# Optimization experiments

Measured on AMD Instinct MI355X. Metric: run time of the kernel, lower is better.

The kernel has to match this reference:

```python
import jax, jax.numpy as jnp
import numpy as np

B, D, IN_F, OUT_F, BLOCK = 2, 1024, 4096, 4096, 128
N_BLOCKS = IN_F // BLOCK  # 32


def setup_inputs() -> dict:
    key = jax.random.key(0)
    k1, k2, k3 = jax.random.split(key, 3)
    inputs = jax.random.normal(k1, (B, D, IN_F), dtype=jnp.float32)
    # int8 quantized weight buffer: [n_blocks, block_size, out_features]
    weight = jax.random.randint(k2, (N_BLOCKS, BLOCK, OUT_F), -128, 128, dtype=jnp.int32).astype(jnp.int8)
    # per-block, per-output-channel scaler: [n_blocks, out_features]
    weight_scaler = (jax.random.uniform(k3, (N_BLOCKS, OUT_F), dtype=jnp.float32) * 0.01 + 0.001)
    return {"inputs": inputs, "weight": weight, "weight_scaler": weight_scaler}


def reference(inputs, weight, weight_scaler):
    # Faithful port of WeightOnlyBlockwiseQuantizedLinear.blockwise_jax_kernel
    # (default path: symmetric quantization, zero_point is None).
    weight = weight.astype(jnp.int8)
    block_size = weight.shape[1]
    b, d, in_f = inputs.shape
    # [b, d, n_blocks s, block_size c]
    x = inputs.reshape(b, d, in_f // block_size, block_size)
    # per-block int8 matmul (promoted to float32 by x): [b, d, s, z]
    out = jnp.einsum("scz,bdsc->bdsz", weight, x)
    # apply per-block scaler and reduce over blocks: [b, d, z]
    out = jnp.einsum("bdsz,sz->bdz", out, weight_scaler)
    return out
```

## Files before the change

### kernel.cpp

```cpp
#include <hip/hip_runtime.h>
#include <hip/hip_bf16.h>


#define MDIM 2048
#define NDIM 4096
#define KDIM 4096
#define NBLK 32
#define BM 128
#define BN 256
#define BK 64
#define NT (KDIM / BK)

typedef __attribute__((ext_vector_type(8))) short bf16x8;
typedef __attribute__((ext_vector_type(4))) float f32x4;
typedef __attribute__((ext_vector_type(8))) unsigned short u16x8;

__device__ __forceinline__ unsigned short f2bf(float f) {
  unsigned u = __float_as_uint(f);
  u += 0x7fffu + ((u >> 16) & 1u);
  return (unsigned short)(u >> 16);
}

__device__ __forceinline__ void gl_lds16(const void* g, void* l) {
  __builtin_amdgcn_global_load_lds(
      (const __attribute__((address_space(1))) unsigned int*)g,
      (__attribute__((address_space(3))) unsigned int*)l,
      16, 0, 0);
}

__global__ void prep_a_kernel(const float* __restrict__ x,
                              unsigned short* __restrict__ ab) {
  int i = blockIdx.x * blockDim.x + threadIdx.x;
  const float4 v = reinterpret_cast<const float4*>(x)[i];
  ushort4 hv;
  hv.x = f2bf(v.x); hv.y = f2bf(v.y); hv.z = f2bf(v.z); hv.w = f2bf(v.w);
  reinterpret_cast<ushort4*>(ab)[i] = hv;
}

__global__ void prep_b_kernel(const int* __restrict__ w,
                              const float* __restrict__ scaler,
                              unsigned short* __restrict__ bt) {
  __shared__ __align__(16) unsigned short tile[64][72];
  const int t = threadIdx.x;
  const int k0 = blockIdx.y * 64;
  const int n0 = blockIdx.x * 64;
  const int s = k0 >> 7;
  {
    const int kl = t >> 2;
    const int nb = t & 3;
    const int nbase = n0 + nb * 16;
    const int4* src = reinterpret_cast<const int4*>(w + (size_t)(k0 + kl) * NDIM + nbase);
    const float4* scv = reinterpret_cast<const float4*>(scaler + (size_t)s * NDIM + nbase);
#pragma unroll
    for (int q = 0; q < 4; ++q) {
      const int4 v = src[q];
      const float4 sc = scv[q];
      const int rbase = nb * 16 + q * 4;
      const int swzr = ((rbase >> 3) & 7) << 3;
      const int ckl = kl ^ swzr;
      tile[rbase + 0][ckl] = f2bf((float)v.x * sc.x);
      tile[rbase + 1][ckl] = f2bf((float)v.y * sc.y);
      tile[rbase + 2][ckl] = f2bf((float)v.z * sc.z);
      tile[rbase + 3][ckl] = f2bf((float)v.w * sc.w);
    }
  }
  __syncthreads();
  {
    const int nl = t >> 2;
    const int swzn = (nl >> 3) & 7;
#pragma unroll
    for (int q = 0; q < 2; ++q) {
      const int ch = (t & 3) * 2 + q;
      u16x8 v = *reinterpret_cast<const u16x8*>(&tile[nl][(ch ^ swzn) * 8]);
      *reinterpret_cast<u16x8*>(bt + (size_t)(n0 + nl) * KDIM + k0 + ch * 8) = v;
    }
  }
}

#define MFMA_BF16 __builtin_amdgcn_mfma_f32_16x16x32_bf16

__global__ __launch_bounds__(512, 2)
void gemm_kernel(const unsigned short* __restrict__ ab,
                 const unsigned short* __restrict__ bt,
                 float* __restrict__ out) {
  __shared__ __align__(16) char lds[98304];

  const int t = threadIdx.x;
  const int lane = t & 63;
  const int wid = t >> 6;
  const int wm = wid >> 2;
  const int wn = wid & 3;
  const int lane15 = lane & 15;
  const int laneq = lane >> 4;
  const int swz = (lane & 7) << 4;

  const unsigned flat = blockIdx.x;
  const unsigned swzb = (flat & 7u) * 32u + (flat >> 3);
  const int ntile = swzb & 15;
  const int mtile = swzb >> 4;
  const int m0 = mtile * BM;
  const int n0 = ntile * BN;

  const int srow = t >> 3;
  const int sslot = (t & 7) ^ (srow & 7);
  const char* ga = (const char*)ab + ((size_t)(m0 + srow) * KDIM) * 2 + sslot * 16;
  const char* gb = (const char*)bt + ((size_t)(n0 + srow) * KDIM) * 2 + sslot * 16;
  const size_t rstep = (size_t)64 * KDIM * 2;

  char* const lA0 = lds + (size_t)wid * 1024;
  char* const lB0 = lds + 32768 + (size_t)wid * 1024;

#define STAGE(kt, c) do {                                   \
    const size_t ko_ = (size_t)(kt) * (BK * 2);             \
    char* a_ = lA0 + (c) * 16384;                           \
    char* b_ = lB0 + (c) * 32768;                           \
    gl_lds16(ga + ko_,             a_);                     \
    gl_lds16(ga + ko_ + rstep,     a_ + 8192);              \
    gl_lds16(gb + ko_,             b_);                     \
    gl_lds16(gb + ko_ + rstep,     b_ + 8192);              \
    gl_lds16(gb + ko_ + 2 * rstep, b_ + 16384);             \
    gl_lds16(gb + ko_ + 3 * rstep, b_ + 24576);             \
  } while (0)

  int offA[4], offB[4];
#pragma unroll
  for (int i = 0; i < 4; ++i) {
    offA[i] = (wm * 64 + i * 16 + lane15) * 128 + laneq * 16;
    offB[i] = (wn * 64 + i * 16 + lane15) * 128 + laneq * 16;
  }

  const f32x4 fzero = {0.f, 0.f, 0.f, 0.f};
  f32x4 acc[4][4];
#pragma unroll
  for (int m = 0; m < 4; ++m)
#pragma unroll
    for (int n = 0; n < 4; ++n) acc[m][n] = fzero;

  STAGE(0, 0);
  STAGE(1, 1);
  asm volatile("s_waitcnt vmcnt(6)" ::: "memory");
  __builtin_amdgcn_s_barrier();

#define LDA(m, base) do {                                             \
    af[m][0] = *(const bf16x8*)((base) + ((offA[m]) ^ swz));          \
    af[m][1] = *(const bf16x8*)((base) + ((offA[m] + 64) ^ swz));     \
  } while (0)
#define LDB(n, base) do {                                             \
    bfr[n][0] = *(const bf16x8*)((base) + ((offB[n]) ^ swz));         \
    bfr[n][1] = *(const bf16x8*)((base) + ((offB[n] + 64) ^ swz));    \
  } while (0)
#define QUAD(mA, mB, nA, nB) do {                                     \
    __builtin_amdgcn_s_setprio(1);                                    \
    acc[mA][nA] = MFMA_BF16(af[mA][0], bfr[nA][0], acc[mA][nA], 0, 0, 0); \
    acc[mA][nB] = MFMA_BF16(af[mA][0], bfr[nB][0], acc[mA][nB], 0, 0, 0); \
    acc[mB][nA] = MFMA_BF16(af[mB][0], bfr[nA][0], acc[mB][nA], 0, 0, 0); \
    acc[mB][nB] = MFMA_BF16(af[mB][0], bfr[nB][0], acc[mB][nB], 0, 0, 0); \
    acc[mA][nA] = MFMA_BF16(af[mA][1], bfr[nA][1], acc[mA][nA], 0, 0, 0); \
    acc[mA][nB] = MFMA_BF16(af[mA][1], bfr[nB][1], acc[mA][nB], 0, 0, 0); \
    acc[mB][nA] = MFMA_BF16(af[mB][1], bfr[nA][1], acc[mB][nA], 0, 0, 0); \
    acc[mB][nB] = MFMA_BF16(af[mB][1], bfr[nB][1], acc[mB][nB], 0, 0, 0); \
    __builtin_amdgcn_s_setprio(0);                                    \
  } while (0)

#pragma unroll 2
  for (int t2 = 0; t2 < NT; ++t2) {
    const int c = t2 & 1;
    const char* lac = lds + c * 16384;
    const char* lbc = lds + 32768 + c * 32768;
    bf16x8 af[4][2], bfr[4][2];

    LDA(0, lac); LDA(1, lac); LDB(0, lbc); LDB(1, lbc);
    __builtin_amdgcn_s_barrier();
    QUAD(0, 1, 0, 1);
    __builtin_amdgcn_s_barrier();

    LDB(2, lbc); LDB(3, lbc);
    __builtin_amdgcn_s_barrier();
    QUAD(0, 1, 2, 3);
    __builtin_amdgcn_s_barrier();

    LDA(2, lac); LDA(3, lac);
    __builtin_amdgcn_s_barrier();
    QUAD(2, 3, 2, 3);
    __builtin_amdgcn_s_barrier();
    __builtin_amdgcn_sched_barrier(0);

    if (t2 + 2 < NT) STAGE(t2 + 2, c);
    QUAD(2, 3, 0, 1);
    if (t2 + 2 < NT) {
      asm volatile("s_waitcnt vmcnt(6)" ::: "memory");
    } else {
      asm volatile("s_waitcnt vmcnt(0)" ::: "memory");
    }
    __builtin_amdgcn_s_barrier();
  }

#pragma unroll
  for (int m = 0; m < 4; ++m)
#pragma unroll
    for (int r = 0; r < 4; ++r) {
      const int row = m0 + wm * 64 + m * 16 + laneq * 4 + r;
      float* op = out + (size_t)row * NDIM + n0 + wn * 64 + lane15;
#pragma unroll
      for (int n = 0; n < 4; ++n) op[n * 16] = acc[m][n][r];
    }
#undef STAGE
#undef LDA
#undef LDB
#undef QUAD
}

__global__ void fallback_kernel(const float* __restrict__ x,
                                const int* __restrict__ w,
                                const float* __restrict__ scaler,
                                float* __restrict__ out) {
  const int n = blockIdx.x * 256 + threadIdx.x;
  const int m = blockIdx.y;
  float acc = 0.f;
  for (int s = 0; s < NBLK; ++s) {
    float p = 0.f;
    const float* xr = x + (size_t)m * KDIM + s * 128;
    const int* wr = w + (size_t)s * 128 * NDIM + n;
#pragma unroll 8
    for (int c = 0; c < 128; ++c) p += xr[c] * (float)wr[(size_t)c * NDIM];
    acc += p * scaler[s * NDIM + n];
  }
  out[(size_t)m * NDIM + n] = acc;
}

extern "C" void kernel_launch(void* const* d_in, const int* in_sizes, int n_in,
                              void* d_out, int out_size, void* d_ws, size_t ws_size,
                              hipStream_t stream) {
  (void)in_sizes; (void)n_in; (void)out_size;
  const float* x = (const float*)d_in[0];
  const int* w = (const int*)d_in[1];
  const float* sc = (const float*)d_in[2];
  float* out = (float*)d_out;

  const size_t need = (size_t)51 * 1024 * 1024;
  if (ws_size >= need) {
    unsigned short* ab = (unsigned short*)d_ws;
    unsigned short* bt = ab + (size_t)MDIM * KDIM;
    prep_a_kernel<<<(MDIM * KDIM / 4) / 256, 256, 0, stream>>>(x, ab);
    prep_b_kernel<<<dim3(NDIM / 64, KDIM / 64), 256, 0, stream>>>(w, sc, bt);
    gemm_kernel<<<(MDIM / BM) * (NDIM / BN), 512, 0, stream>>>(ab, bt, out);
  } else {
    fallback_kernel<<<dim3(NDIM / 256, MDIM), 256, 0, stream>>>(x, w, sc, out);
  }
}
```

Before: 203.8 us.

## Register-transpose weight prep and software-pipeline LDS fragment loads in GEMM

```diff
diff --git a/kernel.cpp b/kernel.cpp
--- a/kernel.cpp
+++ b/kernel.cpp
@@ -40,41 +40,32 @@
 __global__ void prep_b_kernel(const int* __restrict__ w,
                               const float* __restrict__ scaler,
                               unsigned short* __restrict__ bt) {
-  __shared__ __align__(16) unsigned short tile[64][72];
   const int t = threadIdx.x;
-  const int k0 = blockIdx.y * 64;
-  const int n0 = blockIdx.x * 64;
-  const int s = k0 >> 7;
+  const int n0 = blockIdx.x * 128;
+  const int k0 = blockIdx.y * 128;
+  const int s = blockIdx.y;
+  const int k8 = (t & 15) * 8;
+  const int n8 = (t >> 4) * 8;
+
+  float sc[8];
   {
-    const int kl = t >> 2;
-    const int nb = t & 3;
-    const int nbase = n0 + nb * 16;
-    const int4* src = reinterpret_cast<const int4*>(w + (size_t)(k0 + kl) * NDIM + nbase);
-    const float4* scv = reinterpret_cast<const float4*>(scaler + (size_t)s * NDIM + nbase);
-#pragma unroll
-    for (int q = 0; q < 4; ++q) {
-      const int4 v = src[q];
-      const float4 sc = scv[q];
-      const int rbase = nb * 16 + q * 4;
-      const int swzr = ((rbase >> 3) & 7) << 3;
-      const int ckl = kl ^ swzr;
-      tile[rbase + 0][ckl] = f2bf((float)v.x * sc.x);
-      tile[rbase + 1][ckl] = f2bf((float)v.y * sc.y);
-      tile[rbase + 2][ckl] = f2bf((float)v.z * sc.z);
-      tile[rbase + 3][ckl] = f2bf((float)v.w * sc.w);
-    }
-  }
-  __syncthreads();
-  {
-    const int nl = t >> 2;
-    const int swzn = (nl >> 3) & 7;
-#pragma unroll
-    for (int q = 0; q < 2; ++q) {
-      const int ch = (t & 3) * 2 + q;
-      u16x8 v = *reinterpret_cast<const u16x8*>(&tile[nl][(ch ^ swzn) * 8]);
-      *reinterpret_cast<u16x8*>(bt + (size_t)(n0 + nl) * KDIM + k0 + ch * 8) = v;
-    }
-  }
+    const float4* scv = reinterpret_cast<const float4*>(scaler + (size_t)s * NDIM + n0 + n8);
+    const float4 s0 = scv[0], s1 = scv[1];
+    sc[0] = s0.x; sc[1] = s0.y; sc[2] = s0.z; sc[3] = s0.w;
+    sc[4] = s1.x; sc[5] = s1.y; sc[6] = s1.z; sc[7] = s1.w;
+  }
+  u16x8 outv[8];
+#pragma unroll
+  for (int r = 0; r < 8; ++r) {
+    const int4* src = reinterpret_cast<const int4*>(w + (size_t)(k0 + k8 + r) * NDIM + n0 + n8);
+    const int4 a = src[0], b = src[1];
+    const int v[8] = {a.x, a.y, a.z, a.w, b.x, b.y, b.z, b.w};
+#pragma unroll
+    for (int j = 0; j < 8; ++j) outv[j][r] = f2bf((float)v[j] * sc[j]);
+  }
+#pragma unroll
+  for (int j = 0; j < 8; ++j)
+    *reinterpret_cast<u16x8*>(bt + (size_t)(n0 + n8 + j) * KDIM + k0 + k8) = outv[j];
 }
 
 #define MFMA_BF16 __builtin_amdgcn_mfma_f32_16x16x32_bf16
@@ -136,63 +127,82 @@
 #pragma unroll
     for (int n = 0; n < 4; ++n) acc[m][n] = fzero;
 
+  bf16x8 af[4][2];
+  bf16x8 bfr[2][4][2];
+
+#define LDA(m, base) do {                                             \
+    af[m][0] = *(const bf16x8*)((base) + ((offA[m]) ^ swz));          \
+    af[m][1] = *(const bf16x8*)((base) + ((offA[m] + 64) ^ swz));     \
+  } while (0)
+#define LDB(S, n, base) do {                                          \
+    bfr[S][n][0] = *(const bf16x8*)((base) + ((offB[n]) ^ swz));      \
+    bfr[S][n][1] = *(const bf16x8*)((base) + ((offB[n] + 64) ^ swz)); \
+  } while (0)
+#define HALF(mA, mB, P) do {                                               \
+    acc[mA][0] = MFMA_BF16(af[mA][0], bfr[P][0][0], acc[mA][0], 0, 0, 0);  \
+    acc[mA][1] = MFMA_BF16(af[mA][0], bfr[P][1][0], acc[mA][1], 0, 0, 0);  \
+    acc[mA][2] = MFMA_BF16(af[mA][0], bfr[P][2][0], acc[mA][2], 0, 0, 0);  \
+    acc[mA][3] = MFMA_BF16(af[mA][0], bfr[P][3][0], acc[mA][3], 0, 0, 0);  \
+    acc[mB][0] = MFMA_BF16(af[mB][0], bfr[P][0][0], acc[mB][0], 0, 0, 0);  \
+    acc[mB][1] = MFMA_BF16(af[mB][0], bfr[P][1][0], acc[mB][1], 0, 0, 0);  \
+    acc[mB][2] = MFMA_BF16(af[mB][0], bfr[P][2][0], acc[mB][2], 0, 0, 0);  \
+    acc[mB][3] = MFMA_BF16(af[mB][0], bfr[P][3][0], acc[mB][3], 0, 0, 0);  \
+    acc[mA][0] = MFMA_BF16(af[mA][1], bfr[P][0][1], acc[mA][0], 0, 0, 0);  \
+    acc[mA][1] = MFMA_BF16(af[mA][1], bfr[P][1][1], acc[mA][1], 0, 0, 0);  \
+    acc[mA][2] = MFMA_BF16(af[mA][1], bfr[P][2][1], acc[mA][2], 0, 0, 0);  \
+    acc[mA][3] = MFMA_BF16(af[mA][1], bfr[P][3][1], acc[mA][3], 0, 0, 0);  \
+    acc[mB][0] = MFMA_BF16(af[mB][1], bfr[P][0][1], acc[mB][0], 0, 0, 0);  \
+    acc[mB][1] = MFMA_BF16(af[mB][1], bfr[P][1][1], acc[mB][1], 0, 0, 0);  \
+    acc[mB][2] = MFMA_BF16(af[mB][1], bfr[P][2][1], acc[mB][2], 0, 0, 0);  \
+    acc[mB][3] = MFMA_BF16(af[mB][1], bfr[P][3][1], acc[mB][3], 0, 0, 0);  \
+  } while (0)
+
+#define BODY(t2, P) do {                                                   \
+    char* lac = lds + (P) * 16384;                                         \
+                                                        \
+    LDA(2, lac); LDA(3, lac);                                              \
+    __builtin_amdgcn_s_barrier();                                          \
+    __builtin_amdgcn_s_setprio(1);                                         \
+    HALF(0, 1, P);                                                         \
+    __builtin_amdgcn_s_setprio(0);                                         \
+    asm volatile("s_waitcnt lgkmcnt(0)" ::: "memory"); \
+    __builtin_amdgcn_s_barrier();                                          \
+                                                        \
+    if ((t2) + 2 < NT) {                                                   \
+      STAGE((t2) + 2, P);                                                  \
+      asm volatile("s_waitcnt vmcnt(6)" ::: "memory");    \
+    } else {                                                               \
+      asm volatile("s_waitcnt vmcnt(0)" ::: "memory");                     \
+    }                                                                      \
+    __builtin_amdgcn_s_barrier();                                          \
+    __builtin_amdgcn_sched_barrier(0);                                     \
+    if ((t2) + 1 < NT) {                                                   \
+      char* nac = lds + (1 - (P)) * 16384;                                 \
+      char* nbc = lds + 32768 + (1 - (P)) * 32768;                         \
+      LDA(0, nac); LDA(1, nac);                                            \
+      LDB(1 - (P), 0, nbc); LDB(1 - (P), 1, nbc);                          \
+      LDB(1 - (P), 2, nbc); LDB(1 - (P), 3, nbc);                          \
+    }                                                                      \
+    __builtin_amdgcn_s_setprio(1);                                         \
+    HALF(2, 3, P);                                                         \
+    __builtin_amdgcn_s_setprio(0);                                         \
+    __builtin_amdgcn_s_barrier();                                          \
+  } while (0)
+
   STAGE(0, 0);
   STAGE(1, 1);
   asm volatile("s_waitcnt vmcnt(6)" ::: "memory");
   __builtin_amdgcn_s_barrier();
-
-#define LDA(m, base) do {                                             \
-    af[m][0] = *(const bf16x8*)((base) + ((offA[m]) ^ swz));          \
-    af[m][1] = *(const bf16x8*)((base) + ((offA[m] + 64) ^ swz));     \
-  } while (0)
-#define LDB(n, base) do {                                             \
-    bfr[n][0] = *(const bf16x8*)((base) + ((offB[n]) ^ swz));         \
-    bfr[n][1] = *(const bf16x8*)((base) + ((offB[n] + 64) ^ swz));    \
-  } while (0)
-#define QUAD(mA, mB, nA, nB) do {                                     \
-    __builtin_amdgcn_s_setprio(1);                                    \
-    acc[mA][nA] = MFMA_BF16(af[mA][0], bfr[nA][0], acc[mA][nA], 0, 0, 0); \
-    acc[mA][nB] = MFMA_BF16(af[mA][0], bfr[nB][0], acc[mA][nB], 0, 0, 0); \
-    acc[mB][nA] = MFMA_BF16(af[mB][0], bfr[nA][0], acc[mB][nA], 0, 0, 0); \
-    acc[mB][nB] = MFMA_BF16(af[mB][0], bfr[nB][0], acc[mB][nB], 0, 0, 0); \
-    acc[mA][nA] = MFMA_BF16(af[mA][1], bfr[nA][1], acc[mA][nA], 0, 0, 0); \
-    acc[mA][nB] = MFMA_BF16(af[mA][1], bfr[nB][1], acc[mA][nB], 0, 0, 0); \
-    acc[mB][nA] = MFMA_BF16(af[mB][1], bfr[nA][1], acc[mB][nA], 0, 0, 0); \
-    acc[mB][nB] = MFMA_BF16(af[mB][1], bfr[nB][1], acc[mB][nB], 0, 0, 0); \
-    __builtin_amdgcn_s_setprio(0);                                    \
-  } while (0)
-
-#pragma unroll 2
-  for (int t2 = 0; t2 < NT; ++t2) {
-    const int c = t2 & 1;
-    const char* lac = lds + c * 16384;
-    const char* lbc = lds + 32768 + c * 32768;
-    bf16x8 af[4][2], bfr[4][2];
-
-    LDA(0, lac); LDA(1, lac); LDB(0, lbc); LDB(1, lbc);
-    __builtin_amdgcn_s_barrier();
-    QUAD(0, 1, 0, 1);
-    __builtin_amdgcn_s_barrier();
-
-    LDB(2, lbc); LDB(3, lbc);
-    __builtin_amdgcn_s_barrier();
-    QUAD(0, 1, 2, 3);
-    __builtin_amdgcn_s_barrier();
-
-    LDA(2, lac); LDA(3, lac);
-    __builtin_amdgcn_s_barrier();
-    QUAD(2, 3, 2, 3);
-    __builtin_amdgcn_s_barrier();
-    __builtin_amdgcn_sched_barrier(0);
-
-    if (t2 + 2 < NT) STAGE(t2 + 2, c);
-    QUAD(2, 3, 0, 1);
-    if (t2 + 2 < NT) {
-      asm volatile("s_waitcnt vmcnt(6)" ::: "memory");
-    } else {
-      asm volatile("s_waitcnt vmcnt(0)" ::: "memory");
-    }
-    __builtin_amdgcn_s_barrier();
+  {
+    char* nac = lds;
+    char* nbc = lds + 32768;
+    LDA(0, nac); LDA(1, nac);
+    LDB(0, 0, nbc); LDB(0, 1, nbc); LDB(0, 2, nbc); LDB(0, 3, nbc);
+  }
+
+  for (int t2 = 0; t2 < NT; t2 += 2) {
+    BODY(t2, 0);
+    BODY(t2 + 1, 1);
   }
 
 #pragma unroll
@@ -207,7 +217,8 @@
 #undef STAGE
 #undef LDA
 #undef LDB
-#undef QUAD
+#undef HALF
+#undef BODY
 }
 
 __global__ void fallback_kernel(const float* __restrict__ x,
@@ -242,7 +253,7 @@
     unsigned short* ab = (unsigned short*)d_ws;
     unsigned short* bt = ab + (size_t)MDIM * KDIM;
     prep_a_kernel<<<(MDIM * KDIM / 4) / 256, 256, 0, stream>>>(x, ab);
-    prep_b_kernel<<<dim3(NDIM / 64, KDIM / 64), 256, 0, stream>>>(w, sc, bt);
+    prep_b_kernel<<<dim3(NDIM / 128, KDIM / 128), 256, 0, stream>>>(w, sc, bt);
     gemm_kernel<<<(MDIM / BM) * (NDIM / BN), 512, 0, stream>>>(ab, bt, out);
   } else {
     fallback_kernel<<<dim3(NDIM / 256, MDIM), 256, 0, stream>>>(x, w, sc, out);
```

Result: slower. 208.1 us (+2.1%).
